# Kernel tuning notes

Hardware: AMD Instinct MI355X
Metric: run time of the kernel (lower is better)

Reference implementation:

```python
import jax, jax.numpy as jnp
import numpy as np

NEG_SLOPE = 0.2
EPS = 1e-16  # PyG softmax eps


def _gat_conv(x, src, dst, W, att_src, att_dst, bias, heads, out_ch):
    """PyG GATConv (eval mode, self-loops already appended, concat output)."""
    N = x.shape[0]
    xw = (x @ W).reshape(N, heads, out_ch)            # [N,H,C]
    a_src = jnp.sum(xw * att_src, axis=-1)            # [N,H]
    a_dst = jnp.sum(xw * att_dst, axis=-1)            # [N,H]
    e = jax.nn.leaky_relu(a_src[src] + a_dst[dst], NEG_SLOPE)  # [E,H]
    m = jax.ops.segment_max(e, dst, num_segments=N)   # [N,H] (self-loops -> no empty segs)
    e = jnp.exp(e - m[dst])
    denom = jax.ops.segment_sum(e, dst, num_segments=N)
    alpha = e / (denom[dst] + EPS)                    # [E,H]
    msg = xw[src] * alpha[:, :, None]                 # [E,H,C]
    out = jax.ops.segment_sum(msg, dst, num_segments=N)  # [N,H,C]
    return out.reshape(N, heads * out_ch) + bias


def setup_inputs() -> dict:
    key = jax.random.key(0)
    ks = jax.random.split(key, 12)
    N, E, F_in, H, C, NC = 20000, 320000, 512, 8, 64, 32
    x = jax.random.normal(ks[0], (N, F_in), dtype=jnp.float32)
    edge_index = jax.random.randint(ks[1], (2, E), 0, N, dtype=jnp.int64)
    g = lambda k, shape, fan: jax.random.normal(k, shape, dtype=jnp.float32) * (1.0 / np.sqrt(fan))
    return {
        "x": x,
        "edge_index": edge_index,
        "W1": g(ks[2], (F_in, H * C), F_in),
        "att_src1": g(ks[3], (H, C), C),
        "att_dst1": g(ks[4], (H, C), C),
        "b1": jnp.zeros((H * C,), dtype=jnp.float32),
        "W2": g(ks[5], (H * C, NC), H * C),
        "att_src2": g(ks[6], (1, NC), NC),
        "att_dst2": g(ks[7], (1, NC), NC),
        "b2": jnp.zeros((NC,), dtype=jnp.float32),
    }


def reference(x, edge_index, W1, att_src1, att_dst1, b1, W2, att_src2, att_dst2, b2):
    N = x.shape[0]
    H, C = att_src1.shape
    NC = att_src2.shape[1]
    # GATConv adds self-loops by default
    loops = jnp.arange(N, dtype=edge_index.dtype)
    src = jnp.concatenate([edge_index[0], loops])
    dst = jnp.concatenate([edge_index[1], loops])
    h = _gat_conv(x, src, dst, W1, att_src1, att_dst1, b1, H, C)
    h = jax.nn.elu(h)
    h = _gat_conv(h, src, dst, W2, att_src2, att_dst2, b2, 1, NC)
    return jax.nn.log_softmax(h, axis=1)
```

## Files before the change

kernel.cpp:

```cpp
#include <hip/hip_runtime.h>
#include <math.h>

#define NEG_SLOPE 0.2f
#define SM_EPS 1e-16f

typedef short short8 __attribute__((ext_vector_type(8)));
typedef float floatx4 __attribute__((ext_vector_type(4)));


__device__ inline unsigned short f2bf(float x) {
    unsigned int u = __float_as_uint(x);
    unsigned int r = (u + 0x7FFFu + ((u >> 16) & 1u)) >> 16;
    return (unsigned short)r;
}

__device__ inline float bf2f(unsigned short h) {
    return __uint_as_float(((unsigned int)h) << 16);
}

__device__ inline float bflo(unsigned int u) { return __uint_as_float(u << 16); }
__device__ inline float bfhi(unsigned int u) { return __uint_as_float(u & 0xFFFF0000u); }

__device__ __forceinline__ void gl_lds16(const unsigned short* g, unsigned short* l) {
    __builtin_amdgcn_global_load_lds(
        (const __attribute__((address_space(1))) unsigned int*)(g),
        (__attribute__((address_space(3))) unsigned int*)(l), 16, 0, 0);
}

__device__ inline void get_edge(const int* __restrict__ srcA, const int* __restrict__ dstA,
                                int e, int E, int& s, int& d) {
    if (e < E) { s = srcA[e]; d = dstA[e]; }
    else { s = e - E; d = e - E; }
}


__global__ __launch_bounds__(256) void k_cast_x(const float* __restrict__ x,
                                                unsigned short* __restrict__ xb, int nblk_x,
                                                const float* __restrict__ W2,
                                                unsigned short* __restrict__ w2bt) {
    int bx = blockIdx.x;
    if (bx < nblk_x) {
        int i = (bx * 256 + threadIdx.x) * 4;
        float4 v = *(const float4*)(x + i);
        ushort4 o;
        o.x = f2bf(v.x); o.y = f2bf(v.y); o.z = f2bf(v.z); o.w = f2bf(v.w);
        *(ushort4*)(xb + i) = o;
    } else {
        int i = (bx - nblk_x) * 256 + threadIdx.x;
        int c = i >> 9, k = i & 511;
        w2bt[i] = f2bf(W2[k * 32 + c]);
    }
}

__global__ __launch_bounds__(256) void k_cast_w1t(const float* __restrict__ W,
                                                  unsigned short* __restrict__ Wt) {
    __shared__ float tile[32][33];
    int bx = blockIdx.x * 32;
    int by = blockIdx.y * 32;
    int tx = threadIdx.x & 31, ty = threadIdx.x >> 5;
    #pragma unroll
    for (int i = 0; i < 32; i += 8)
        tile[ty + i][tx] = W[(size_t)(bx + ty + i) * 512 + by + tx];
    __syncthreads();
    #pragma unroll
    for (int i = 0; i < 32; i += 8)
        Wt[(size_t)(by + ty + i) * 512 + bx + tx] = f2bf(tile[tx][ty + i]);
}


__global__ __launch_bounds__(256) void k_deg(const int* __restrict__ dstA, int E, int Ep,
                                             int* __restrict__ deg) {
    int e = blockIdx.x * 256 + threadIdx.x;
    if (e >= Ep) return;
    int d = (e < E) ? dstA[e] : (e - E);
    atomicAdd(&deg[d], 1);
}

__global__ __launch_bounds__(256) void k_scan1(const int* __restrict__ deg, int* __restrict__ incl,
                                               int* __restrict__ part, int N) {
    __shared__ int sm[256];
    int t = threadIdx.x;
    int i = blockIdx.x * 256 + t;
    int v = (i < N) ? deg[i] : 0;
    sm[t] = v; __syncthreads();
    for (int o = 1; o < 256; o <<= 1) {
        int x = (t >= o) ? sm[t - o] : 0;
        __syncthreads();
        sm[t] += x;
        __syncthreads();
    }
    if (i < N) incl[i] = sm[t];
    if (t == 255) part[blockIdx.x] = sm[255];
}

__global__ __launch_bounds__(256) void k_scan3(const int* __restrict__ incl, const int* __restrict__ part,
                                               const int* __restrict__ deg, int* __restrict__ off,
                                               int* __restrict__ cursor, int N) {
    __shared__ int sm[256];
    int bx = blockIdx.x, t = threadIdx.x;
    int partial = 0;
    for (int i = t; i < bx; i += 256) partial += part[i];
    sm[t] = partial; __syncthreads();
    for (int o = 128; o > 0; o >>= 1) {
        if (t < o) sm[t] += sm[t + o];
        __syncthreads();
    }
    int base = sm[0];
    int i = bx * 256 + t;
    if (i >= N) return;
    int v = incl[i] + base;
    off[i + 1] = v;
    cursor[i] = v - deg[i];
    if (i == 0) off[0] = 0;
}

__global__ __launch_bounds__(256) void k_scatter(const int* __restrict__ srcA, const int* __restrict__ dstA,
                                                 int E, int Ep, int* __restrict__ cursor,
                                                 int* __restrict__ src_s) {
    int e = blockIdx.x * 256 + threadIdx.x;
    if (e >= Ep) return;
    int s, d; get_edge(srcA, dstA, e, E, s, d);
    int p = atomicAdd(&cursor[d], 1);
    src_s[p] = s;
}


__global__ __launch_bounds__(256) void k_gemm1_mfma(const unsigned short* __restrict__ A,
                                                    const unsigned short* __restrict__ Bt,
                                                    const float* __restrict__ att_s,
                                                    const float* __restrict__ att_d,
                                                    unsigned short* __restrict__ C,
                                                    float* __restrict__ a_sd,
                                                    float* __restrict__ a_dd, int M) {
    const int K = 512;
    __shared__ unsigned short As[128 * 32];
    __shared__ unsigned short Bs[128 * 32];
    int t = threadIdx.x;
    int lane = t & 63;
    int w = t >> 6;
    int row0 = blockIdx.x * 128;
    int col0 = blockIdx.y * 128;
    int wm = (w >> 1) * 64, wn = (w & 1) * 64;
    int l15 = lane & 15, q = lane >> 4;

    int mrow = t >> 2;
    int kk = (t & 3) * 8;
    unsigned short* ldsA0 = &As[w * 512];
    unsigned short* ldsA1 = &As[2048 + w * 512];
    unsigned short* ldsB0 = &Bs[w * 512];
    unsigned short* ldsB1 = &Bs[2048 + w * 512];

    floatx4 acc[4][4] = {};

    for (int k0 = 0; k0 < K; k0 += 32) {
        gl_lds16(A  + (size_t)(row0 + mrow) * K + k0 + kk,      ldsA0);
        gl_lds16(A  + (size_t)(row0 + 64 + mrow) * K + k0 + kk, ldsA1);
        gl_lds16(Bt + (size_t)(col0 + mrow) * K + k0 + kk,      ldsB0);
        gl_lds16(Bt + (size_t)(col0 + 64 + mrow) * K + k0 + kk, ldsB1);
        __syncthreads();
        short8 af[4], bfr[4];
        #pragma unroll
        for (int i = 0; i < 4; ++i)
            af[i] = *(const short8*)(&As[(wm + i * 16 + l15) * 32 + q * 8]);
        #pragma unroll
        for (int j = 0; j < 4; ++j)
            bfr[j] = *(const short8*)(&Bs[(wn + j * 16 + l15) * 32 + q * 8]);
        #pragma unroll
        for (int i = 0; i < 4; ++i)
            #pragma unroll
            for (int j = 0; j < 4; ++j)
                acc[i][j] = __builtin_amdgcn_mfma_f32_16x16x32_bf16(af[i], bfr[j], acc[i][j], 0, 0, 0);
        __syncthreads();
    }

    #pragma unroll
    for (int i = 0; i < 4; ++i) {
        #pragma unroll
        for (int p = 0; p < 4; ++p) {
            int r = row0 + wm + i * 16 + q * 4 + p;
            if (r < M) {
                #pragma unroll
                for (int j = 0; j < 4; ++j) {
                    int c = col0 + wn + j * 16 + l15;
                    C[(size_t)r * 512 + c] = f2bf(acc[i][j][p]);
                }
            }
        }
    }

    int hh = blockIdx.y * 2 + (w & 1);
    float asr[4], adr[4];
    #pragma unroll
    for (int j = 0; j < 4; ++j) {
        asr[j] = att_s[hh * 64 + j * 16 + l15];
        adr[j] = att_d[hh * 64 + j * 16 + l15];
    }
    #pragma unroll
    for (int i = 0; i < 4; ++i) {
        #pragma unroll
        for (int p = 0; p < 4; ++p) {
            float ds = 0.f, dd = 0.f;
            #pragma unroll
            for (int j = 0; j < 4; ++j) {
                ds = fmaf(acc[i][j][p], asr[j], ds);
                dd = fmaf(acc[i][j][p], adr[j], dd);
            }
            #pragma unroll
            for (int mk = 1; mk <= 8; mk <<= 1) {
                ds += __shfl_xor(ds, mk);
                dd += __shfl_xor(dd, mk);
            }
            int r = row0 + wm + i * 16 + q * 4 + p;
            if (l15 == 0 && r < M) {
                a_sd[r * 8 + hh] = ds;
                a_dd[r * 8 + hh] = dd;
            }
        }
    }
}


__global__ __launch_bounds__(256) void k_l1(const unsigned short* __restrict__ xw,
                                            const float* __restrict__ a_s,
                                            const float* __restrict__ a_d,
                                            const int* __restrict__ off,
                                            const int* __restrict__ src_s,
                                            const float* __restrict__ bias,
                                            unsigned short* __restrict__ hout, int N) {
    int wid = threadIdx.x >> 6, lane = threadIdx.x & 63;
    int n = blockIdx.x * 4 + wid;
    if (n >= N) return;
    int p0 = off[n], p1 = off[n + 1];
    int q = lane >> 3;
    int be = lane >> 3;
    int bh = lane & 7;
    float adb = a_d[n * 8 + bh];
    const size_t cbase = (size_t)8 * lane;

    float acc[8] = {};
    float s = 0.f;
    int p = p0;
    for (; p + 8 <= p1; p += 8) {
        int bsrc = src_s[p + be];
        float e = a_s[bsrc * 8 + bh] + adb;
        e = e > 0.f ? e : NEG_SLOPE * e;
        float w8 = __expf(e);
        #pragma unroll
        for (int j = 0; j < 8; ++j) {
            int sj = __shfl(bsrc, j * 8);
            float wj = __shfl(w8, j * 8 + q);
            const uint4 u = *(const uint4*)(xw + (size_t)sj * 512 + cbase);
            s += wj;
            acc[0] = fmaf(wj, bflo(u.x), acc[0]); acc[1] = fmaf(wj, bfhi(u.x), acc[1]);
            acc[2] = fmaf(wj, bflo(u.y), acc[2]); acc[3] = fmaf(wj, bfhi(u.y), acc[3]);
            acc[4] = fmaf(wj, bflo(u.z), acc[4]); acc[5] = fmaf(wj, bfhi(u.z), acc[5]);
            acc[6] = fmaf(wj, bflo(u.w), acc[6]); acc[7] = fmaf(wj, bfhi(u.w), acc[7]);
        }
    }
    if (p < p1) {
        int nb = p1 - p;
        int bsrc = src_s[p + (be < nb ? be : 0)];
        float e = a_s[bsrc * 8 + bh] + adb;
        e = e > 0.f ? e : NEG_SLOPE * e;
        float w8 = __expf(e);
        for (int j = 0; j < nb; ++j) {
            int sj = __shfl(bsrc, j * 8);
            float wj = __shfl(w8, j * 8 + q);
            const uint4 u = *(const uint4*)(xw + (size_t)sj * 512 + cbase);
            s += wj;
            acc[0] = fmaf(wj, bflo(u.x), acc[0]); acc[1] = fmaf(wj, bfhi(u.x), acc[1]);
            acc[2] = fmaf(wj, bflo(u.y), acc[2]); acc[3] = fmaf(wj, bfhi(u.y), acc[3]);
            acc[4] = fmaf(wj, bflo(u.z), acc[4]); acc[5] = fmaf(wj, bfhi(u.z), acc[5]);
            acc[6] = fmaf(wj, bflo(u.w), acc[6]); acc[7] = fmaf(wj, bfhi(u.w), acc[7]);
        }
    }

    float inv = 1.f / (s + SM_EPS);
    unsigned int ov[4];
    #pragma unroll
    for (int j = 0; j < 4; ++j) {
        float v0 = acc[2 * j] * inv     + bias[cbase + 2 * j];
        float v1 = acc[2 * j + 1] * inv + bias[cbase + 2 * j + 1];
        v0 = v0 > 0.f ? v0 : expm1f(v0);
        v1 = v1 > 0.f ? v1 : expm1f(v1);
        ov[j] = (unsigned int)f2bf(v0) | ((unsigned int)f2bf(v1) << 16);
    }
    *(uint4*)(hout + (size_t)n * 512 + cbase) = make_uint4(ov[0], ov[1], ov[2], ov[3]);
}


__global__ __launch_bounds__(256) void k_gemm2_mfma(const unsigned short* __restrict__ A,
                                                    const unsigned short* __restrict__ Bt,
                                                    const float* __restrict__ att_s,
                                                    const float* __restrict__ att_d,
                                                    unsigned short* __restrict__ O,
                                                    float* __restrict__ a_s, float* __restrict__ a_d,
                                                    int M) {
    const int K = 512;
    __shared__ unsigned short As[64 * 40];
    __shared__ unsigned short Bs[32 * 40];
    int t = threadIdx.x;
    int lane = t & 63;
    int w = t >> 6;
    int row0 = blockIdx.x * 64;
    int l15 = lane & 15, q = lane >> 4;

    floatx4 acc[2] = {};

    for (int k0 = 0; k0 < K; k0 += 32) {
        {
            int flat = t * 8;
            int m = flat >> 5, kk = flat & 31;
            uint4 va = make_uint4(0u, 0u, 0u, 0u);
            int gr = row0 + m;
            if (gr < M) va = *(const uint4*)(A + (size_t)gr * K + k0 + kk);
            *(uint4*)(&As[m * 40 + kk]) = va;
            if (t < 128) {
                int nn = t >> 2, kb = (t & 3) * 8;
                *(uint4*)(&Bs[nn * 40 + kb]) = *(const uint4*)(Bt + (size_t)nn * K + k0 + kb);
            }
        }
        __syncthreads();
        short8 af = *(const short8*)(&As[(w * 16 + l15) * 40 + q * 8]);
        short8 b0 = *(const short8*)(&Bs[(l15) * 40 + q * 8]);
        short8 b1 = *(const short8*)(&Bs[(16 + l15) * 40 + q * 8]);
        acc[0] = __builtin_amdgcn_mfma_f32_16x16x32_bf16(af, b0, acc[0], 0, 0, 0);
        acc[1] = __builtin_amdgcn_mfma_f32_16x16x32_bf16(af, b1, acc[1], 0, 0, 0);
        __syncthreads();
    }

    float as_lo = att_s[l15], as_hi = att_s[16 + l15];
    float ad_lo = att_d[l15], ad_hi = att_d[16 + l15];
    #pragma unroll
    for (int p = 0; p < 4; ++p) {
        int r = row0 + w * 16 + q * 4 + p;
        bool ok = r < M;
        float v0 = acc[0][p], v1 = acc[1][p];
        if (ok) {
            O[(size_t)r * 32 + l15]      = f2bf(v0);
            O[(size_t)r * 32 + 16 + l15] = f2bf(v1);
        }
        float ds = v0 * as_lo + v1 * as_hi;
        float dd = v0 * ad_lo + v1 * ad_hi;
        #pragma unroll
        for (int mk = 1; mk <= 8; mk <<= 1) {
            ds += __shfl_xor(ds, mk);
            dd += __shfl_xor(dd, mk);
        }
        if (ok && l15 == 0) { a_s[r] = ds; a_d[r] = dd; }
    }
}


__global__ __launch_bounds__(256) void k_l2(const unsigned short* __restrict__ hw2,
                                            const float* __restrict__ a_s,
                                            const float* __restrict__ a_d,
                                            const int* __restrict__ off,
                                            const int* __restrict__ src_s,
                                            const float* __restrict__ bias,
                                            float* __restrict__ outp, int N) {
    int wid = threadIdx.x >> 6, lane = threadIdx.x & 63;
    int n = blockIdx.x * 4 + wid;
    if (n >= N) return;
    int p0 = off[n], p1 = off[n + 1];
    float adv = a_d[n];
    int c = lane & 31, ep = lane >> 5;

    float acc = 0.f, s = 0.f;
    int p = p0;
    for (; p + 64 <= p1; p += 64) {
        int bsrc = src_s[p + lane];
        float e = a_s[bsrc] + adv;
        e = e > 0.f ? e : NEG_SLOPE * e;
        float w64 = __expf(e);
        #pragma unroll
        for (int j = 0; j < 64; j += 2) {
            int sj = __shfl(bsrc, j + ep);
            float wj = __shfl(w64, j + ep);
            s += wj;
            acc = fmaf(wj, bf2f(hw2[(size_t)sj * 32 + c]), acc);
        }
    }
    if (p < p1) {
        int nb = p1 - p;
        int bsrc = src_s[p + (lane < nb ? lane : 0)];
        float e = a_s[bsrc] + adv;
        e = e > 0.f ? e : NEG_SLOPE * e;
        float w64 = __expf(e);
        for (int j = 0; j < nb; j += 2) {
            int idx = j + ep;
            bool valid = idx < nb;
            int idc = valid ? idx : 0;
            int sj = __shfl(bsrc, idc);
            float wj = __shfl(w64, idc);
            if (valid) {
                s += wj;
                acc = fmaf(wj, bf2f(hw2[(size_t)sj * 32 + c]), acc);
            }
        }
    }
    acc += __shfl_xor(acc, 32);
    s   += __shfl_xor(s, 32);
    float v = acc / (s + SM_EPS) + bias[c];
    float mx = v;
    #pragma unroll
    for (int mk = 16; mk >= 1; mk >>= 1) mx = fmaxf(mx, __shfl_xor(mx, mk, 32));
    float ex = __expf(v - mx);
    float sum = ex;
    #pragma unroll
    for (int mk = 16; mk >= 1; mk >>= 1) sum += __shfl_xor(sum, mk, 32);
    if (lane < 32) outp[(size_t)n * 32 + c] = (v - mx) - __logf(sum);
}


extern "C" void kernel_launch(void* const* d_in, const int* in_sizes, int n_in,
                              void* d_out, int out_size, void* d_ws, size_t ws_size,
                              hipStream_t stream) {
    const float* x   = (const float*)d_in[0];
    const int*   ei  = (const int*)d_in[1];
    const float* W1  = (const float*)d_in[2];
    const float* as1 = (const float*)d_in[3];
    const float* ad1 = (const float*)d_in[4];
    const float* b1  = (const float*)d_in[5];
    const float* W2  = (const float*)d_in[6];
    const float* as2 = (const float*)d_in[7];
    const float* ad2 = (const float*)d_in[8];
    const float* b2  = (const float*)d_in[9];
    float* out = (float*)d_out;

    const int F = 512;
    const int N = in_sizes[0] / F;
    const int E = in_sizes[1] / 2;
    const int Ep = E + N;
    const int* srcA = ei;
    const int* dstA = ei + E;

    char* w = (char*)d_ws;
    auto alloc = [&](size_t b) -> void* {
        void* p = (void*)w;
        w += (b + 255) & ~(size_t)255;
        return p;
    };
    unsigned short* xbf  = (unsigned short*)alloc((size_t)N * 512 * 2);
    unsigned short* w1t  = (unsigned short*)alloc((size_t)512 * 512 * 2);
    unsigned short* w2bt = (unsigned short*)alloc((size_t)32 * 512 * 2);
    unsigned short* xw1  = (unsigned short*)alloc((size_t)N * 512 * 2);
    unsigned short* hbuf = (unsigned short*)alloc((size_t)N * 512 * 2);
    float* a_s1 = (float*)alloc((size_t)N * 8 * 4);
    float* a_d1 = (float*)alloc((size_t)N * 8 * 4);
    unsigned short* hw2 = (unsigned short*)alloc((size_t)N * 32 * 2);
    float* a_s2 = (float*)alloc((size_t)N * 4);
    float* a_d2 = (float*)alloc((size_t)N * 4);
    int* deg    = (int*)alloc((size_t)N * 4);
    int* incl   = (int*)alloc((size_t)N * 4);
    int* part   = (int*)alloc(256 * 4);
    int* off    = (int*)alloc((size_t)(N + 1) * 4);
    int* cursor = (int*)alloc((size_t)N * 4);
    int* src_s  = (int*)alloc((size_t)Ep * 4);

    int egrid = (Ep + 255) / 256;
    int sgrid = (N + 255) / 256;
    int ngrid4 = (N + 3) / 4;
    int nblk_x = (N * 512 / 4) / 256;
    int nblk_w2 = (32 * 512 + 255) / 256;

    hipMemsetAsync(deg, 0, (size_t)N * 4, stream);

    k_cast_x<<<nblk_x + nblk_w2, 256, 0, stream>>>(x, xbf, nblk_x, W2, w2bt);
    {
        dim3 gt(16, 16);
        k_cast_w1t<<<gt, 256, 0, stream>>>(W1, w1t);
    }

    k_deg<<<egrid, 256, 0, stream>>>(dstA, E, Ep, deg);
    k_scan1<<<sgrid, 256, 0, stream>>>(deg, incl, part, N);
    k_scan3<<<sgrid, 256, 0, stream>>>(incl, part, deg, off, cursor, N);
    k_scatter<<<egrid, 256, 0, stream>>>(srcA, dstA, E, Ep, cursor, src_s);

    {
        dim3 g1((N + 127) / 128, 512 / 128);
        k_gemm1_mfma<<<g1, 256, 0, stream>>>(xbf, w1t, as1, ad1, xw1, a_s1, a_d1, N);
    }
    k_l1<<<ngrid4, 256, 0, stream>>>(xw1, a_s1, a_d1, off, src_s, b1, hbuf, N);

    k_gemm2_mfma<<<(N + 63) / 64, 256, 0, stream>>>(hbuf, w2bt, as2, ad2, hw2, a_s2, a_d2, N);
    k_l2<<<ngrid4, 256, 0, stream>>>(hw2, a_s2, a_d2, off, src_s, b2, out, N);
}
```

Baseline: 265.6 us.

## Split layer-1 aggregation per head and parallelize edges across lane groups

The layer-1 aggregation kernel now assigns one wavefront to each (node, head) pair instead of one wavefront per node. Within the wave, eight groups of eight lanes each take different edges at the same time, with two edges per group per iteration. Each group recomputes its own attention weight, and the partial sums are combined at the end with cross-lane shuffles. The aim is to issue more independent gathers at once and so hide memory latency in this gather-heavy, latency-bound loop. The cost is an eight-times larger grid, repeated loads of the node's offsets and attention scalars, and the extra shuffle reduction.

New measurement: 305.2 us. +14.9%, slower.

```diff
diff --git a/kernel.cpp b/kernel.cpp
--- a/kernel.cpp
+++ b/kernel.cpp
@@ -228,64 +228,71 @@
                                             const float* __restrict__ bias,
                                             unsigned short* __restrict__ hout, int N) {
     int wid = threadIdx.x >> 6, lane = threadIdx.x & 63;
-    int n = blockIdx.x * 4 + wid;
+    int h = blockIdx.x & 7;
+    int n = (blockIdx.x >> 3) * 4 + wid;
     if (n >= N) return;
     int p0 = off[n], p1 = off[n + 1];
-    int q = lane >> 3;
-    int be = lane >> 3;
-    int bh = lane & 7;
-    float adb = a_d[n * 8 + bh];
-    const size_t cbase = (size_t)8 * lane;
+    int g = lane >> 3;
+    int li = lane & 7;
+    float adv = a_d[n * 8 + h];
+    const size_t cbase = (size_t)h * 64 + (size_t)li * 8;
 
     float acc[8] = {};
     float s = 0.f;
-    int p = p0;
-    for (; p + 8 <= p1; p += 8) {
-        int bsrc = src_s[p + be];
-        float e = a_s[bsrc * 8 + bh] + adb;
-        e = e > 0.f ? e : NEG_SLOPE * e;
-        float w8 = __expf(e);
-        #pragma unroll
-        for (int j = 0; j < 8; ++j) {
-            int sj = __shfl(bsrc, j * 8);
-            float wj = __shfl(w8, j * 8 + q);
-            const uint4 u = *(const uint4*)(xw + (size_t)sj * 512 + cbase);
-            s += wj;
-            acc[0] = fmaf(wj, bflo(u.x), acc[0]); acc[1] = fmaf(wj, bfhi(u.x), acc[1]);
-            acc[2] = fmaf(wj, bflo(u.y), acc[2]); acc[3] = fmaf(wj, bfhi(u.y), acc[3]);
-            acc[4] = fmaf(wj, bflo(u.z), acc[4]); acc[5] = fmaf(wj, bfhi(u.z), acc[5]);
-            acc[6] = fmaf(wj, bflo(u.w), acc[6]); acc[7] = fmaf(wj, bfhi(u.w), acc[7]);
-        }
+    int p = p0 + g;
+    for (; p + 8 < p1; p += 16) {
+        int s0 = src_s[p];
+        int s1 = src_s[p + 8];
+        const uint4 u0 = *(const uint4*)(xw + (size_t)s0 * 512 + cbase);
+        const uint4 u1 = *(const uint4*)(xw + (size_t)s1 * 512 + cbase);
+        float e0 = a_s[s0 * 8 + h] + adv; e0 = e0 > 0.f ? e0 : NEG_SLOPE * e0;
+        float e1 = a_s[s1 * 8 + h] + adv; e1 = e1 > 0.f ? e1 : NEG_SLOPE * e1;
+        float w0 = __expf(e0);
+        float w1 = __expf(e1);
+        s += w0 + w1;
+        acc[0] = fmaf(w0, bflo(u0.x), acc[0]); acc[1] = fmaf(w0, bfhi(u0.x), acc[1]);
+        acc[2] = fmaf(w0, bflo(u0.y), acc[2]); acc[3] = fmaf(w0, bfhi(u0.y), acc[3]);
+        acc[4] = fmaf(w0, bflo(u0.z), acc[4]); acc[5] = fmaf(w0, bfhi(u0.z), acc[5]);
+        acc[6] = fmaf(w0, bflo(u0.w), acc[6]); acc[7] = fmaf(w0, bfhi(u0.w), acc[7]);
+        acc[0] = fmaf(w1, bflo(u1.x), acc[0]); acc[1] = fmaf(w1, bfhi(u1.x), acc[1]);
+        acc[2] = fmaf(w1, bflo(u1.y), acc[2]); acc[3] = fmaf(w1, bfhi(u1.y), acc[3]);
+        acc[4] = fmaf(w1, bflo(u1.z), acc[4]); acc[5] = fmaf(w1, bfhi(u1.z), acc[5]);
+        acc[6] = fmaf(w1, bflo(u1.w), acc[6]); acc[7] = fmaf(w1, bfhi(u1.w), acc[7]);
     }
     if (p < p1) {
-        int nb = p1 - p;
-        int bsrc = src_s[p + (be < nb ? be : 0)];
-        float e = a_s[bsrc * 8 + bh] + adb;
-        e = e > 0.f ? e : NEG_SLOPE * e;
-        float w8 = __expf(e);
-        for (int j = 0; j < nb; ++j) {
-            int sj = __shfl(bsrc, j * 8);
-            float wj = __shfl(w8, j * 8 + q);
-            const uint4 u = *(const uint4*)(xw + (size_t)sj * 512 + cbase);
-            s += wj;
-            acc[0] = fmaf(wj, bflo(u.x), acc[0]); acc[1] = fmaf(wj, bfhi(u.x), acc[1]);
-            acc[2] = fmaf(wj, bflo(u.y), acc[2]); acc[3] = fmaf(wj, bfhi(u.y), acc[3]);
-            acc[4] = fmaf(wj, bflo(u.z), acc[4]); acc[5] = fmaf(wj, bfhi(u.z), acc[5]);
-            acc[6] = fmaf(wj, bflo(u.w), acc[6]); acc[7] = fmaf(wj, bfhi(u.w), acc[7]);
-        }
-    }
-
-    float inv = 1.f / (s + SM_EPS);
-    unsigned int ov[4];
-    #pragma unroll
-    for (int j = 0; j < 4; ++j) {
-        float v0 = acc[2 * j] * inv     + bias[cbase + 2 * j];
-        float v1 = acc[2 * j + 1] * inv + bias[cbase + 2 * j + 1];
-        v0 = v0 > 0.f ? v0 : expm1f(v0);
-        v1 = v1 > 0.f ? v1 : expm1f(v1);
-        ov[j] = (unsigned int)f2bf(v0) | ((unsigned int)f2bf(v1) << 16);
-    }
-    *(uint4*)(hout + (size_t)n * 512 + cbase) = make_uint4(ov[0], ov[1], ov[2], ov[3]);
+        int s0 = src_s[p];
+        const uint4 u0 = *(const uint4*)(xw + (size_t)s0 * 512 + cbase);
+        float e0 = a_s[s0 * 8 + h] + adv; e0 = e0 > 0.f ? e0 : NEG_SLOPE * e0;
+        float w0 = __expf(e0);
+        s += w0;
+        acc[0] = fmaf(w0, bflo(u0.x), acc[0]); acc[1] = fmaf(w0, bfhi(u0.x), acc[1]);
+        acc[2] = fmaf(w0, bflo(u0.y), acc[2]); acc[3] = fmaf(w0, bfhi(u0.y), acc[3]);
+        acc[4] = fmaf(w0, bflo(u0.z), acc[4]); acc[5] = fmaf(w0, bfhi(u0.z), acc[5]);
+        acc[6] = fmaf(w0, bflo(u0.w), acc[6]); acc[7] = fmaf(w0, bfhi(u0.w), acc[7]);
+    }
+
+    #pragma unroll
+    for (int mk = 1; mk <= 32; mk <<= 1) s += __shfl_xor(s, mk);
+    s *= 0.125f;
+    #pragma unroll
+    for (int mk = 8; mk <= 32; mk <<= 1) {
+        #pragma unroll
+        for (int i = 0; i < 8; ++i) acc[i] += __shfl_xor(acc[i], mk);
+    }
+
+    if (g == 0) {
+        float inv = 1.f / (s + SM_EPS);
+        unsigned int ov[4];
+        #pragma unroll
+        for (int j = 0; j < 4; ++j) {
+            float v0 = acc[2 * j] * inv     + bias[cbase + 2 * j];
+            float v1 = acc[2 * j + 1] * inv + bias[cbase + 2 * j + 1];
+            v0 = v0 > 0.f ? v0 : expm1f(v0);
+            v1 = v1 > 0.f ? v1 : expm1f(v1);
+            ov[j] = (unsigned int)f2bf(v0) | ((unsigned int)f2bf(v1) << 16);
+        }
+        *(uint4*)(hout + (size_t)n * 512 + cbase) = make_uint4(ov[0], ov[1], ov[2], ov[3]);
+    }
 }
 
 
@@ -481,7 +488,7 @@
         dim3 g1((N + 127) / 128, 512 / 128);
         k_gemm1_mfma<<<g1, 256, 0, stream>>>(xbf, w1t, as1, ad1, xw1, a_s1, a_d1, N);
     }
-    k_l1<<<ngrid4, 256, 0, stream>>>(xw1, a_s1, a_d1, off, src_s, b1, hbuf, N);
+    k_l1<<<ngrid4 * 8, 256, 0, stream>>>(xw1, a_s1, a_d1, off, src_s, b1, hbuf, N);
 
     k_gemm2_mfma<<<(N + 63) / 64, 256, 0, stream>>>(hbuf, w2bt, as2, ad2, hw2, a_s2, a_d2, N);
     k_l2<<<ngrid4, 256, 0, stream>>>(hw2, a_s2, a_d2, off, src_s, b2, out, N);
```
